# Kernel tuning notes

Hardware: AMD Instinct MI355X
Metric: run time of the kernel (lower is better)

## Reference

```python
import jax, jax.numpy as jnp
import numpy as np

B, S, D, T, H = 4, 2048, 1024, 5, 8


def setup_inputs() -> dict:
    key = jax.random.key(0)
    ks = jax.random.split(key, 12)
    sc = 0.02  # small init scale for weights so attention logits stay sane
    return {
        "x": jax.random.normal(ks[0], (B, S, D), jnp.float32),
        "time_steps": jax.random.randint(ks[1], (B, S), 0, T),
        "gamma": jnp.ones((T, D), jnp.float32),
        "beta": jax.random.normal(ks[2], (T, D), jnp.float32) * sc,
        "decay": jnp.ones((T,), jnp.float32),
        "shift_W": jax.random.normal(ks[3], (D, D), jnp.float32) * sc,
        "shift_b": jax.random.normal(ks[4], (D,), jnp.float32) * sc,
        "in_proj_W": jax.random.normal(ks[5], (3 * D, D), jnp.float32) * sc,
        "in_proj_b": jax.random.normal(ks[6], (3 * D,), jnp.float32) * sc,
        "out_proj_W": jax.random.normal(ks[7], (D, D), jnp.float32) * sc,
        "out_proj_b": jax.random.normal(ks[8], (D,), jnp.float32) * sc,
    }


def reference(x, time_steps, gamma, beta, decay, shift_W, shift_b,
              in_proj_W, in_proj_b, out_proj_W, out_proj_b):
    eps = 1e-5
    T_ = gamma.shape[0]
    b_, s_, d_ = x.shape
    hd = d_ // H

    # --- per-token indexed LayerNorm + decay (vectorized gather of norm params) ---
    idx = jnp.clip(time_steps, 0, T_ - 1)              # safe gather index [B,S]
    mu = jnp.mean(x, axis=-1, keepdims=True)
    var = jnp.mean(jnp.square(x - mu), axis=-1, keepdims=True)
    xn = (x - mu) * jax.lax.rsqrt(var + eps)           # [B,S,D]
    normed = (xn * gamma[idx] + beta[idx]) * decay[idx][..., None]
    x = jnp.where((time_steps < T_)[..., None], normed, x)

    # --- residual temporal shift (Linear) ---
    x = x + x @ shift_W.T + shift_b

    # --- torch-style MultiheadAttention(x, x, x), batch_first ---
    qkv = x @ in_proj_W.T + in_proj_b                  # [B,S,3D]
    q, k, v = jnp.split(qkv, 3, axis=-1)
    q = q.reshape(b_, s_, H, hd)
    k = k.reshape(b_, s_, H, hd)
    v = v.reshape(b_, s_, H, hd)
    scale = 1.0 / jnp.sqrt(jnp.asarray(hd, x.dtype))
    scores = jnp.einsum('bqhd,bkhd->bhqk', q, k) * scale   # [B,H,S,S]
    attn = jax.nn.softmax(scores, axis=-1)
    ctx = jnp.einsum('bhqk,bkhd->bqhd', attn, v).reshape(b_, s_, d_)
    attended = ctx @ out_proj_W.T + out_proj_b
    return x + attended
```

## Files before the change

kernel.cpp:

```cpp
#include <hip/hip_runtime.h>
#include <math.h>

#define B_ 4
#define S_ 2048
#define D_ 1024
#define T_ 5
#define H_ 8
#define HD_ 128
#define M_ (B_*S_)

typedef __bf16 bf16x8 __attribute__((ext_vector_type(8)));
typedef float  f32x4  __attribute__((ext_vector_type(4)));

__device__ __forceinline__ float bf2f(unsigned short u) {
    union { unsigned int i; float f; } c; c.i = ((unsigned int)u) << 16; return c.f;
}
__device__ __forceinline__ unsigned short f2bf(float f) {
    union { float f; unsigned int i; } c; c.f = f;
    unsigned int u = c.i;
    u += 0x7fffu + ((u >> 16) & 1u);
    return (unsigned short)(u >> 16);
}

__device__ __forceinline__ void gll16(const void* g, void* l) {
    __builtin_amdgcn_global_load_lds(
        (const __attribute__((address_space(1))) void*)g,
        (__attribute__((address_space(3))) void*)l, 16, 0, 0);
}

__global__ __launch_bounds__(256) void f2bf3_kernel(
    const float* __restrict__ s0,
    const float* __restrict__ s1,
    const float* __restrict__ s2,
    unsigned short* __restrict__ dst)
{
    int i = (blockIdx.x * 256 + threadIdx.x) * 4;
    const float* src;
    int local;
    if (i < D_ * D_)              { src = s0; local = i; }
    else if (i < 4 * D_ * D_)     { src = s1; local = i - D_ * D_; }
    else                          { src = s2; local = i - 4 * D_ * D_; }
    float4 v = *(const float4*)(src + local);
    ushort4 o;
    o.x = f2bf(v.x); o.y = f2bf(v.y); o.z = f2bf(v.z); o.w = f2bf(v.w);
    *(ushort4*)(dst + i) = o;
}

__global__ __launch_bounds__(256) void ln_kernel(
    const float* __restrict__ x, const int* __restrict__ ts,
    const float* __restrict__ gamma, const float* __restrict__ beta,
    const float* __restrict__ decay, unsigned short* __restrict__ out)
{
    int row = blockIdx.x;
    int tid = threadIdx.x;
    float4 v = ((const float4*)(x + (size_t)row * D_))[tid];
    float s  = v.x + v.y + v.z + v.w;
    float s2 = v.x*v.x + v.y*v.y + v.z*v.z + v.w*v.w;
    #pragma unroll
    for (int off = 32; off; off >>= 1) {
        s  += __shfl_down(s,  off);
        s2 += __shfl_down(s2, off);
    }
    __shared__ float ps[4], ps2[4];
    if ((tid & 63) == 0) { ps[tid >> 6] = s; ps2[tid >> 6] = s2; }
    __syncthreads();
    float tot  = ps[0]  + ps[1]  + ps[2]  + ps[3];
    float tot2 = ps2[0] + ps2[1] + ps2[2] + ps2[3];
    float mu   = tot  * (1.0f / D_);
    float var  = tot2 * (1.0f / D_) - mu * mu;
    float rstd = rsqrtf(var + 1e-5f);

    int t  = ts[row];
    int tc = min(max(t, 0), T_ - 1);
    float4 g = ((const float4*)(gamma + (size_t)tc * D_))[tid];
    float4 b = ((const float4*)(beta  + (size_t)tc * D_))[tid];
    float dec = decay[tc];

    float4 o;
    o.x = ((v.x - mu) * rstd * g.x + b.x) * dec;
    o.y = ((v.y - mu) * rstd * g.y + b.y) * dec;
    o.z = ((v.z - mu) * rstd * g.z + b.z) * dec;
    o.w = ((v.w - mu) * rstd * g.w + b.w) * dec;
    if (t >= T_) o = v;
    ushort4 ob;
    ob.x = f2bf(o.x); ob.y = f2bf(o.y); ob.z = f2bf(o.z); ob.w = f2bf(o.w);
    ((ushort4*)(out + (size_t)row * D_))[tid] = ob;
}

__global__ __launch_bounds__(256) void gemm_mfma(
    const unsigned short* __restrict__ A,
    const unsigned short* __restrict__ Wt,
    const float* __restrict__ bias,
    const float* __restrict__ ResF,
    const unsigned short* __restrict__ ResB,
    float* __restrict__ Cf,
    unsigned short* __restrict__ Cb,
    int M, int N, int K)
{
    __shared__ __align__(16) unsigned short As[128 * 32];
    __shared__ __align__(16) unsigned short Bs[128 * 32];
    int tid  = threadIdx.x;
    int w    = tid >> 6, lane = tid & 63;
    int lm   = lane & 15, quad = lane >> 4;
    int wm   = w & 1,  wn   = w >> 1;

    int nwgx  = gridDim.x;
    int lin   = blockIdx.y * nwgx + blockIdx.x;
    int chunk = (nwgx * gridDim.y) >> 3;
    int swz   = (lin & 7) * chunk + (lin >> 3);
    int bx    = swz % nwgx, by = swz / nwgx;

    int i0 = by * 128, j0 = bx * 128;

    f32x4 acc[4][4];
    #pragma unroll
    for (int mt = 0; mt < 4; ++mt)
        #pragma unroll
        for (int nt = 0; nt < 4; ++nt)
            acc[mt][nt] = (f32x4){0.f, 0.f, 0.f, 0.f};

    int c0 = w * 128 + lane;
    int r0 = c0 >> 2,   k80 = (c0 & 3) * 8;
    int c1 = c0 + 64;
    int r1 = c1 >> 2,   k81 = (c1 & 3) * 8;

    for (int kt = 0; kt < K; kt += 32) {
        __syncthreads();
        gll16(A  + (size_t)(i0 + r0) * K + kt + k80, As + (size_t)(w * 128 + 0 ) * 8);
        gll16(A  + (size_t)(i0 + r1) * K + kt + k81, As + (size_t)(w * 128 + 64) * 8);
        gll16(Wt + (size_t)(j0 + r0) * K + kt + k80, Bs + (size_t)(w * 128 + 0 ) * 8);
        gll16(Wt + (size_t)(j0 + r1) * K + kt + k81, Bs + (size_t)(w * 128 + 64) * 8);
        __syncthreads();

        bf16x8 af[4], bfr[4];
        #pragma unroll
        for (int mt = 0; mt < 4; ++mt)
            af[mt] = *(const bf16x8*)&As[(wm * 64 + mt * 16 + lm) * 32 + quad * 8];
        #pragma unroll
        for (int nt = 0; nt < 4; ++nt)
            bfr[nt] = *(const bf16x8*)&Bs[(wn * 64 + nt * 16 + lm) * 32 + quad * 8];
        #pragma unroll
        for (int mt = 0; mt < 4; ++mt)
            #pragma unroll
            for (int nt = 0; nt < 4; ++nt)
                acc[mt][nt] = __builtin_amdgcn_mfma_f32_16x16x32_bf16(
                    af[mt], bfr[nt], acc[mt][nt], 0, 0, 0);
    }

    #pragma unroll
    for (int nt = 0; nt < 4; ++nt) {
        int j = j0 + wn * 64 + nt * 16 + lm;
        float bj = bias[j];
        #pragma unroll
        for (int mt = 0; mt < 4; ++mt) {
            #pragma unroll
            for (int r = 0; r < 4; ++r) {
                int i = i0 + wm * 64 + mt * 16 + quad * 4 + r;
                size_t off = (size_t)i * N + j;
                float v = acc[mt][nt][r] + bj;
                if (ResF) v += ResF[off];
                else if (ResB) v += bf2f(ResB[off]);
                if (Cf) Cf[off] = v;
                if (Cb) Cb[off] = f2bf(v);
            }
        }
    }
}

__global__ __launch_bounds__(256) void transpose_v(
    const unsigned short* __restrict__ qkv, unsigned short* __restrict__ vt)
{
    __shared__ unsigned short Ts[64][72];
    int t = threadIdx.x;
    int s0 = blockIdx.x * 64, c0 = blockIdx.y * 64, b = blockIdx.z;
    int r  = t >> 2, cg = (t & 3) * 16;
    const unsigned short* src =
        qkv + (size_t)(b * S_ + s0 + r) * (3 * D_) + 2 * D_ + c0 + cg;
    *(bf16x8*)&Ts[r][cg]     = *(const bf16x8*)(src);
    *(bf16x8*)&Ts[r][cg + 8] = *(const bf16x8*)(src + 8);
    __syncthreads();
    int dd = t >> 2, sg = (t & 3) * 16;
    unsigned short tmp[16];
    #pragma unroll
    for (int j = 0; j < 16; ++j) tmp[j] = Ts[sg + j][dd];
    unsigned short* dst = vt + ((size_t)b * D_ + c0 + dd) * S_ + s0 + sg;
    *(bf16x8*)dst       = *(bf16x8*)&tmp[0];
    *(bf16x8*)(dst + 8) = *(bf16x8*)&tmp[8];
}

__global__ __launch_bounds__(256, 2) void flash_mfma(
    const unsigned short* __restrict__ qkv,
    const unsigned short* __restrict__ vt,
    unsigned short* __restrict__ ctx)
{
    __shared__ __align__(16) unsigned short Ks [2][64 * 128];
    __shared__ __align__(16) unsigned short Vts[2][128 * 64];
    __shared__ __align__(16) unsigned short Ps [4][32 * 64];

    int tid  = threadIdx.x;
    int w    = tid >> 6, lane = tid & 63;
    int lm   = lane & 15, quad = lane >> 4;
    int qt = blockIdx.x, h = blockIdx.y, b = blockIdx.z;
    const int rs = 3 * D_;
    const float scale = 0.08838834764831844f;
    size_t qbase  = (size_t)b * S_ * rs + (size_t)h * HD_;
    size_t kbase  = qbase + D_;
    size_t vtbase = ((size_t)b * H_ + h) * (size_t)HD_ * S_;
    int q0 = qt * 128 + w * 32;

    int krow0 = w * 4 + (lane >> 4);
    int kcolE = ((((lane & 15) * 16) ^ ((krow0 & 7) << 4)) >> 1);
    int vrow0 = w * 8 + (lane >> 3);
    int vcolE = ((((lane & 7)  * 16) ^ ((vrow0 & 7) << 4)) >> 1);

    const int rxor = (lm & 7) << 4;

    #pragma unroll
    for (int i = 0; i < 4; ++i) {
        gll16(qkv + kbase + (size_t)(krow0 + 16 * i) * rs + kcolE,
              &Ks[0][i * 2048 + w * 512]);
        gll16(vt  + vtbase + (size_t)(vrow0 + 32 * i) * S_ + vcolE,
              &Vts[0][i * 2048 + w * 512]);
    }

    bf16x8 qf[2][4];
    #pragma unroll
    for (int mt = 0; mt < 2; ++mt)
        #pragma unroll
        for (int kc = 0; kc < 4; ++kc) {
            bf16x8 raw = *(const bf16x8*)(
                qkv + qbase + (size_t)(q0 + mt * 16 + lm) * rs + kc * 32 + quad * 8);
            bf16x8 sc;
            #pragma unroll
            for (int j = 0; j < 8; ++j)
                sc[j] = (__bf16)((float)raw[j] * scale);
            qf[mt][kc] = sc;
        }

    f32x4 oacc[2][8];
    #pragma unroll
    for (int mt = 0; mt < 2; ++mt)
        #pragma unroll
        for (int n = 0; n < 8; ++n)
            oacc[mt][n] = (f32x4){0.f, 0.f, 0.f, 0.f};
    float lst[2][4];
    #pragma unroll
    for (int mt = 0; mt < 2; ++mt)
        #pragma unroll
        for (int r = 0; r < 4; ++r) lst[mt][r] = 0.f;

    int cur = 0;
    for (int kt = 0; kt < S_ / 64; ++kt) {
        __syncthreads();

        if (kt + 1 < S_ / 64) {
            int k0n = (kt + 1) * 64, nb = cur ^ 1;
            #pragma unroll
            for (int i = 0; i < 4; ++i) {
                gll16(qkv + kbase + (size_t)(k0n + krow0 + 16 * i) * rs + kcolE,
                      &Ks[nb][i * 2048 + w * 512]);
                gll16(vt  + vtbase + (size_t)(vrow0 + 32 * i) * S_ + k0n + vcolE,
                      &Vts[nb][i * 2048 + w * 512]);
            }
        }

        const char* Kb = (const char*)&Ks[cur][0];
        const char* Vb = (const char*)&Vts[cur][0];

        f32x4 sacc[2][4];
        #pragma unroll
        for (int mt = 0; mt < 2; ++mt)
            #pragma unroll
            for (int n = 0; n < 4; ++n)
                sacc[mt][n] = (f32x4){0.f, 0.f, 0.f, 0.f};
        __builtin_amdgcn_s_setprio(1);
        #pragma unroll
        for (int n = 0; n < 4; ++n) {
            bf16x8 bk[4];
            #pragma unroll
            for (int kc = 0; kc < 4; ++kc)
                bk[kc] = *(const bf16x8*)(Kb + (n * 16 + lm) * 256 +
                                          ((kc * 64 + quad * 16) ^ rxor));
            #pragma unroll
            for (int mt = 0; mt < 2; ++mt)
                #pragma unroll
                for (int kc = 0; kc < 4; ++kc)
                    sacc[mt][n] = __builtin_amdgcn_mfma_f32_16x16x32_bf16(
                        qf[mt][kc], bk[kc], sacc[mt][n], 0, 0, 0);
        }
        __builtin_amdgcn_s_setprio(0);

        char* Pw = (char*)&Ps[w][0];
        #pragma unroll
        for (int mt = 0; mt < 2; ++mt) {
            #pragma unroll
            for (int r = 0; r < 4; ++r) {
                float p0 = __expf(sacc[mt][0][r]);
                float p1 = __expf(sacc[mt][1][r]);
                float p2 = __expf(sacc[mt][2][r]);
                float p3 = __expf(sacc[mt][3][r]);
                lst[mt][r] += (p0 + p1) + (p2 + p3);
                int row = mt * 16 + quad * 4 + r;
                int wx  = (row & 7) << 4;
                char* rowp = Pw + row * 128;
                *(unsigned short*)(rowp + (( 0 + lm * 2) ^ wx)) = f2bf(p0);
                *(unsigned short*)(rowp + ((32 + lm * 2) ^ wx)) = f2bf(p1);
                *(unsigned short*)(rowp + ((64 + lm * 2) ^ wx)) = f2bf(p2);
                *(unsigned short*)(rowp + ((96 + lm * 2) ^ wx)) = f2bf(p3);
            }
        }

        bf16x8 pa[2][2];
        #pragma unroll
        for (int mt = 0; mt < 2; ++mt)
            #pragma unroll
            for (int kc = 0; kc < 2; ++kc)
                pa[mt][kc] = *(const bf16x8*)(Pw + (mt * 16 + lm) * 128 +
                                              ((kc * 64 + quad * 16) ^ rxor));
        __builtin_amdgcn_s_setprio(1);
        #pragma unroll
        for (int n = 0; n < 8; ++n) {
            bf16x8 bv0 = *(const bf16x8*)(Vb + (n * 16 + lm) * 128 +
                                          (( 0 + quad * 16) ^ rxor));
            bf16x8 bv1 = *(const bf16x8*)(Vb + (n * 16 + lm) * 128 +
                                          ((64 + quad * 16) ^ rxor));
            #pragma unroll
            for (int mt = 0; mt < 2; ++mt) {
                oacc[mt][n] = __builtin_amdgcn_mfma_f32_16x16x32_bf16(
                    pa[mt][0], bv0, oacc[mt][n], 0, 0, 0);
                oacc[mt][n] = __builtin_amdgcn_mfma_f32_16x16x32_bf16(
                    pa[mt][1], bv1, oacc[mt][n], 0, 0, 0);
            }
        }
        __builtin_amdgcn_s_setprio(0);
        cur ^= 1;
    }

    float linv[2][4];
    #pragma unroll
    for (int mt = 0; mt < 2; ++mt)
        #pragma unroll
        for (int r = 0; r < 4; ++r) {
            float l = lst[mt][r];
            l += __shfl_xor(l, 1);
            l += __shfl_xor(l, 2);
            l += __shfl_xor(l, 4);
            l += __shfl_xor(l, 8);
            linv[mt][r] = 1.0f / l;
        }
    size_t rowbase = (size_t)b * S_ + (size_t)qt * 128 + w * 32;
    #pragma unroll
    for (int mt = 0; mt < 2; ++mt)
        #pragma unroll
        for (int r = 0; r < 4; ++r) {
            size_t row = rowbase + mt * 16 + quad * 4 + r;
            unsigned short* dst = ctx + row * D_ + h * HD_ + lm;
            #pragma unroll
            for (int n = 0; n < 8; ++n)
                dst[n * 16] = f2bf(oacc[mt][n][r] * linv[mt][r]);
        }
}

extern "C" void kernel_launch(void* const* d_in, const int* in_sizes, int n_in,
                              void* d_out, int out_size, void* d_ws, size_t ws_size,
                              hipStream_t stream) {
    (void)in_sizes; (void)n_in; (void)out_size; (void)ws_size;
    const float* x          = (const float*)d_in[0];
    const int*   ts         = (const int*)  d_in[1];
    const float* gamma      = (const float*)d_in[2];
    const float* beta       = (const float*)d_in[3];
    const float* decay      = (const float*)d_in[4];
    const float* shift_W    = (const float*)d_in[5];
    const float* shift_b    = (const float*)d_in[6];
    const float* in_proj_W  = (const float*)d_in[7];
    const float* in_proj_b  = (const float*)d_in[8];
    const float* out_proj_W = (const float*)d_in[9];
    const float* out_proj_b = (const float*)d_in[10];
    float* out = (float*)d_out;

    unsigned short* p     = (unsigned short*)d_ws;
    unsigned short* xln_b = p;
    unsigned short* qkv_b = xln_b + (size_t)M_ * D_;
    unsigned short* xs_b  = qkv_b + (size_t)M_ * 3 * D_;
    unsigned short* wsh_b = xs_b  + (size_t)M_ * D_;
    unsigned short* wip_b = wsh_b + (size_t)D_ * D_;
    unsigned short* wop_b = wip_b + (size_t)3 * D_ * D_;
    unsigned short* vt_b  = xs_b;
    unsigned short* ctx_b = xln_b;
    float* xs = out;

    f2bf3_kernel<<<5 * D_ * D_ / 1024, 256, 0, stream>>>(
        shift_W, in_proj_W, out_proj_W, wsh_b);

    ln_kernel<<<M_, 256, 0, stream>>>(x, ts, gamma, beta, decay, xln_b);

    gemm_mfma<<<dim3(D_ / 128, M_ / 128), 256, 0, stream>>>(
        xln_b, wsh_b, shift_b, nullptr, xln_b, xs, xs_b, M_, D_, D_);
    gemm_mfma<<<dim3(3 * D_ / 128, M_ / 128), 256, 0, stream>>>(
        xs_b, wip_b, in_proj_b, nullptr, nullptr, nullptr, qkv_b, M_, 3 * D_, D_);

    transpose_v<<<dim3(S_ / 64, D_ / 64, B_), 256, 0, stream>>>(qkv_b, vt_b);
    flash_mfma<<<dim3(S_ / 128, H_, B_), 256, 0, stream>>>(qkv_b, vt_b, ctx_b);

    gemm_mfma<<<dim3(D_ / 128, M_ / 128), 256, 0, stream>>>(
        ctx_b, wop_b, out_proj_b, xs, nullptr, out, nullptr, M_, D_, D_);
}
```

Baseline: 392.8 us.

## Compute V transposed directly via swapped-operand GEMM, drop transpose kernel

Splits the QKV projection into a Q/K GEMM writing a 2D-wide buffer and a separate GEMM computing V^T = Wv * xs^T, which writes V already transposed in [D, B*S] layout, with a new per-row bias option. This removes the transpose_v kernel and its extra read and write of V. The flash kernel's strides and base offsets are updated to the new layouts. The risk is that the V^T GEMM epilogue writes with stride M per lane and may be less efficient, and there is one extra launch in place of the transpose.

Result: slower. 431.1 us (+9.8%).

```diff
diff --git a/kernel.cpp b/kernel.cpp
--- a/kernel.cpp
+++ b/kernel.cpp
@@ -91,6 +91,7 @@
     const unsigned short* __restrict__ A,
     const unsigned short* __restrict__ Wt,
     const float* __restrict__ bias,
+    const float* __restrict__ biasR,
     const float* __restrict__ ResF,
     const unsigned short* __restrict__ ResB,
     float* __restrict__ Cf,
@@ -150,14 +151,14 @@
     #pragma unroll
     for (int nt = 0; nt < 4; ++nt) {
         int j = j0 + wn * 64 + nt * 16 + lm;
-        float bj = bias[j];
+        float bj = bias ? bias[j] : 0.f;
         #pragma unroll
         for (int mt = 0; mt < 4; ++mt) {
             #pragma unroll
             for (int r = 0; r < 4; ++r) {
                 int i = i0 + wm * 64 + mt * 16 + quad * 4 + r;
                 size_t off = (size_t)i * N + j;
-                float v = acc[mt][nt][r] + bj;
+                float v = acc[mt][nt][r] + (biasR ? biasR[i] : bj);
                 if (ResF) v += ResF[off];
                 else if (ResB) v += bf2f(ResB[off]);
                 if (Cf) Cf[off] = v;
@@ -165,27 +166,6 @@
             }
         }
     }
-}
-
-__global__ __launch_bounds__(256) void transpose_v(
-    const unsigned short* __restrict__ qkv, unsigned short* __restrict__ vt)
-{
-    __shared__ unsigned short Ts[64][72];
-    int t = threadIdx.x;
-    int s0 = blockIdx.x * 64, c0 = blockIdx.y * 64, b = blockIdx.z;
-    int r  = t >> 2, cg = (t & 3) * 16;
-    const unsigned short* src =
-        qkv + (size_t)(b * S_ + s0 + r) * (3 * D_) + 2 * D_ + c0 + cg;
-    *(bf16x8*)&Ts[r][cg]     = *(const bf16x8*)(src);
-    *(bf16x8*)&Ts[r][cg + 8] = *(const bf16x8*)(src + 8);
-    __syncthreads();
-    int dd = t >> 2, sg = (t & 3) * 16;
-    unsigned short tmp[16];
-    #pragma unroll
-    for (int j = 0; j < 16; ++j) tmp[j] = Ts[sg + j][dd];
-    unsigned short* dst = vt + ((size_t)b * D_ + c0 + dd) * S_ + s0 + sg;
-    *(bf16x8*)dst       = *(bf16x8*)&tmp[0];
-    *(bf16x8*)(dst + 8) = *(bf16x8*)&tmp[8];
 }
 
 __global__ __launch_bounds__(256, 2) void flash_mfma(
@@ -201,11 +181,11 @@
     int w    = tid >> 6, lane = tid & 63;
     int lm   = lane & 15, quad = lane >> 4;
     int qt = blockIdx.x, h = blockIdx.y, b = blockIdx.z;
-    const int rs = 3 * D_;
+    const int rs = 2 * D_;
     const float scale = 0.08838834764831844f;
     size_t qbase  = (size_t)b * S_ * rs + (size_t)h * HD_;
     size_t kbase  = qbase + D_;
-    size_t vtbase = ((size_t)b * H_ + h) * (size_t)HD_ * S_;
+    size_t vtbase = (size_t)h * HD_ * M_ + (size_t)b * S_;
     int q0 = qt * 128 + w * 32;
 
     int krow0 = w * 4 + (lane >> 4);
@@ -219,7 +199,7 @@
     for (int i = 0; i < 4; ++i) {
         gll16(qkv + kbase + (size_t)(krow0 + 16 * i) * rs + kcolE,
               &Ks[0][i * 2048 + w * 512]);
-        gll16(vt  + vtbase + (size_t)(vrow0 + 32 * i) * S_ + vcolE,
+        gll16(vt  + vtbase + (size_t)(vrow0 + 32 * i) * M_ + vcolE,
               &Vts[0][i * 2048 + w * 512]);
     }
 
@@ -259,7 +239,7 @@
             for (int i = 0; i < 4; ++i) {
                 gll16(qkv + kbase + (size_t)(k0n + krow0 + 16 * i) * rs + kcolE,
                       &Ks[nb][i * 2048 + w * 512]);
-                gll16(vt  + vtbase + (size_t)(vrow0 + 32 * i) * S_ + k0n + vcolE,
+                gll16(vt  + vtbase + (size_t)(vrow0 + 32 * i) * M_ + k0n + vcolE,
                       &Vts[nb][i * 2048 + w * 512]);
             }
         }
@@ -381,12 +361,12 @@
     unsigned short* p     = (unsigned short*)d_ws;
     unsigned short* xln_b = p;
     unsigned short* qkv_b = xln_b + (size_t)M_ * D_;
-    unsigned short* xs_b  = qkv_b + (size_t)M_ * 3 * D_;
+    unsigned short* xs_b  = qkv_b + (size_t)M_ * 2 * D_;
     unsigned short* wsh_b = xs_b  + (size_t)M_ * D_;
     unsigned short* wip_b = wsh_b + (size_t)D_ * D_;
     unsigned short* wop_b = wip_b + (size_t)3 * D_ * D_;
-    unsigned short* vt_b  = xs_b;
-    unsigned short* ctx_b = xln_b;
+    unsigned short* vt_b  = xln_b;
+    unsigned short* ctx_b = xs_b;
     float* xs = out;
 
     f2bf3_kernel<<<5 * D_ * D_ / 1024, 256, 0, stream>>>(
@@ -395,13 +375,18 @@
     ln_kernel<<<M_, 256, 0, stream>>>(x, ts, gamma, beta, decay, xln_b);
 
     gemm_mfma<<<dim3(D_ / 128, M_ / 128), 256, 0, stream>>>(
-        xln_b, wsh_b, shift_b, nullptr, xln_b, xs, xs_b, M_, D_, D_);
-    gemm_mfma<<<dim3(3 * D_ / 128, M_ / 128), 256, 0, stream>>>(
-        xs_b, wip_b, in_proj_b, nullptr, nullptr, nullptr, qkv_b, M_, 3 * D_, D_);
-
-    transpose_v<<<dim3(S_ / 64, D_ / 64, B_), 256, 0, stream>>>(qkv_b, vt_b);
+        xln_b, wsh_b, shift_b, nullptr, nullptr, xln_b, xs, xs_b, M_, D_, D_);
+
+    gemm_mfma<<<dim3(2 * D_ / 128, M_ / 128), 256, 0, stream>>>(
+        xs_b, wip_b, in_proj_b, nullptr, nullptr, nullptr, nullptr, qkv_b,
+        M_, 2 * D_, D_);
+
+    gemm_mfma<<<dim3(M_ / 128, D_ / 128), 256, 0, stream>>>(
+        wip_b + (size_t)2 * D_ * D_, xs_b, nullptr, in_proj_b + 2 * D_,
+        nullptr, nullptr, nullptr, vt_b, D_, M_, D_);
+
     flash_mfma<<<dim3(S_ / 128, H_, B_), 256, 0, stream>>>(qkv_b, vt_b, ctx_b);
 
     gemm_mfma<<<dim3(D_ / 128, M_ / 128), 256, 0, stream>>>(
-        ctx_b, wop_b, out_proj_b, xs, nullptr, out, nullptr, M_, D_, D_);
-}
+        ctx_b, wop_b, out_proj_b, nullptr, xs, nullptr, out, nullptr, M_, D_, D_);
+}
```
